# Performance work log

Hardware: AMD Instinct MI355X
Metric: run time of the kernel (lower is better)

## Reference

```python
import jax, jax.numpy as jnp
import numpy as np
from jax import lax

EPS = 1e-5


def _poly_ste(x):
    # polynomial STE: forward sign(x), backward piecewise-polynomial surrogate
    s = jnp.sign(x)
    out1 = jnp.where(x < -1.0, -1.0, x * x + 2.0 * x)
    out2 = jnp.where(x < 0.0, out1, -x * x + 2.0 * x)
    out3 = jnp.where(x < 1.0, out2, 1.0)
    return lax.stop_gradient(s - out3) + out3


def _binary_conv(x, w, stride):
    # per-filter scale (detached) * sign(w), STE through clipped weights
    scale = lax.stop_gradient(jnp.mean(jnp.abs(w), axis=(1, 2, 3), keepdims=True))
    wc = jnp.clip(w, -1.0, 1.0)
    bw = lax.stop_gradient(scale * jnp.sign(w) - wc) + wc
    return lax.conv_general_dilated(
        x, bw, window_strides=(stride, stride), padding=[(1, 1), (1, 1)],
        dimension_numbers=('NCHW', 'OIHW', 'NCHW'))


def _bn_train(x, gamma, beta):
    mu = jnp.mean(x, axis=(0, 2, 3), keepdims=True)
    var = jnp.var(x, axis=(0, 2, 3), keepdims=True)  # biased, as torch BN normalization
    return gamma.reshape(1, -1, 1, 1) * (x - mu) * lax.rsqrt(var + EPS) + beta.reshape(1, -1, 1, 1)


def _prelu(x, a):
    a = a.reshape(1, -1, 1, 1)
    return jnp.where(x >= 0, x, a * x)


def setup_inputs() -> dict:
    key = jax.random.key(0)
    ks = jax.random.split(key, 16)
    N, C, H, W = 64, 256, 28, 28
    P = 256  # planes
    d = {}
    d['x'] = jax.random.normal(ks[0], (N, C, H, W), jnp.float32)
    # LearnableBias params (init zeros in torch; small random to exercise math)
    d['b10'] = jax.random.normal(ks[1], (1, C, 1, 1), jnp.float32) * 0.01
    d['w1'] = jax.random.uniform(ks[2], (P, C, 3, 3), jnp.float32) * 0.001
    d['gamma1'] = 1.0 + 0.1 * jax.random.normal(ks[3], (P,), jnp.float32)
    d['beta1'] = 0.1 * jax.random.normal(ks[4], (P,), jnp.float32)
    d['b11'] = jax.random.normal(ks[5], (1, P, 1, 1), jnp.float32) * 0.01
    d['a1'] = 0.25 + 0.01 * jax.random.normal(ks[6], (P,), jnp.float32)
    d['b12'] = jax.random.normal(ks[7], (1, P, 1, 1), jnp.float32) * 0.01
    d['b20'] = jax.random.normal(ks[8], (1, P, 1, 1), jnp.float32) * 0.01
    d['w2'] = jax.random.uniform(ks[9], (P, P, 3, 3), jnp.float32) * 0.001
    d['gamma2'] = 1.0 + 0.1 * jax.random.normal(ks[10], (P,), jnp.float32)
    d['beta2'] = 0.1 * jax.random.normal(ks[11], (P,), jnp.float32)
    d['b21'] = jax.random.normal(ks[12], (1, P, 1, 1), jnp.float32) * 0.01
    d['a2'] = 0.25 + 0.01 * jax.random.normal(ks[13], (P,), jnp.float32)
    d['b22'] = jax.random.normal(ks[14], (1, P, 1, 1), jnp.float32) * 0.01
    return d


def reference(x, b10, w1, gamma1, beta1, b11, a1, b12,
              b20, w2, gamma2, beta2, b21, a2, b22):
    stride = 1
    residual = x
    h = x + b10
    h = _poly_ste(h)
    h = _binary_conv(h, w1, stride)
    h = _bn_train(h, gamma1, beta1)
    h = h + residual
    h = h + b11
    h = _prelu(h, a1)
    h = h + b12
    y = h + b20
    y = _poly_ste(y)
    y = _binary_conv(y, w2, stride)
    y = _bn_train(y, gamma2, beta2)
    y = y + h
    y = y + b21
    y = _prelu(y, a2)
    y = y + b22
    return y
```

## Files before the change

### kernel.cpp

```cpp
#include <hip/hip_runtime.h>

using i32x4 = __attribute__((ext_vector_type(4))) int;

#define OFF_SCALES 0u
#define OFF_AB     4096u
#define OFF_PBUF   8192u
#define OFF_WPK1   925696u
#define OFF_WPK2   1515520u
#define OFF_SPAD   2105344u
#define OFF_COUT   16850944u

__device__ __forceinline__ char sgn8(float v) {
  return v > 0.f ? (char)1 : (v < 0.f ? (char)-1 : (char)0);
}

__global__ __launch_bounds__(256) void k_wprep2(const float* __restrict__ w1,
                                                const float* __restrict__ w2,
                                                char* __restrict__ wp1,
                                                char* __restrict__ wp2,
                                                float* __restrict__ sc) {
  int bid = blockIdx.x;
  int o = bid & 255, c = threadIdx.x;
  const float* w = (bid < 256) ? w1 : w2;
  char* wp = (bid < 256) ? wp1 : wp2;
  const float* wr = w + ((size_t)o * 256 + c) * 9;
  int base = ((c >> 6) * 16384) + ((o >> 4) * 1024) +
             (((o & 15) + (((c >> 4) & 3) << 4)) << 4) + (c & 15);
  float s = 0.f;
#pragma unroll
  for (int khw = 0; khw < 9; ++khw) {
    float v = wr[khw];
    s += fabsf(v);
    wp[khw * 65536 + base] = sgn8(v);
  }
  for (int m = 1; m < 64; m <<= 1) s += __shfl_xor(s, m);
  __shared__ float red[4];
  if ((c & 63) == 0) red[c >> 6] = s;
  __syncthreads();
  if (c == 0) sc[bid] = (red[0] + red[1] + red[2] + red[3]) * (1.f / 2304.f);
}

__global__ __launch_bounds__(512) void k_e0(const float* __restrict__ x,
                                            const float* __restrict__ b10,
                                            char* __restrict__ sp) {
  __shared__ char lds[112 * 260];
  int img = blockIdx.x / 7, y4 = blockIdx.x % 7;
  int y0 = y4 * 4;
  int t = threadIdx.x;
  int r = t & 31;
  int cb = t >> 5;
  if (r < 28) {
    int p0 = r * 4;
    for (int ci = 0; ci < 16; ++ci) {
      int c = ci * 16 + cb;
      float vb = b10[c];
      size_t off = ((size_t)(img * 256 + c) * 28 + y0) * 28 + p0;
      float4 xv = *reinterpret_cast<const float4*>(x + off);
      char* lp = &lds[p0 * 260 + c];
      lp[0]   = sgn8(xv.x + vb);
      lp[260] = sgn8(xv.y + vb);
      lp[520] = sgn8(xv.z + vb);
      lp[780] = sgn8(xv.w + vb);
    }
  }
  __syncthreads();
#pragma unroll
  for (int row = 0; row < 4; ++row) {
    size_t bse = (((size_t)img * 30 + (y0 + row + 1)) * 30 + 1) * 256;
    int* spi = (int*)(sp + bse);
    for (int q = t; q < 1792; q += 512) {
      int xo = q >> 6, c4 = (q & 63) << 2;
      spi[q] = *(const int*)&lds[(row * 28 + xo) * 260 + c4];
    }
  }
  {
    int row = t >> 7, rem = t & 127;
    int col = (rem & 1) * 29, c4w = rem >> 1;
    ((int*)&sp[(((size_t)img * 30 + (y0 + row + 1)) * 30 + col) * 256])[c4w] = 0;
  }
  if (y4 == 0)
    for (int q = t; q < 1920; q += 512)
      ((int*)&sp[(size_t)img * 230400])[q] = 0;
  if (y4 == 6)
    for (int q = t; q < 1920; q += 512)
      ((int*)&sp[(size_t)img * 230400 + 29 * 7680])[q] = 0;
}

__global__ __launch_bounds__(512, 4) void k_conv(const char* __restrict__ S,
                                                 const char* __restrict__ Wp,
                                                 short* __restrict__ C,
                                                 int* __restrict__ P) {
  __shared__ char lds[46080];
  int bid = blockIdx.x;
  int img = bid / 7;
  int yt  = bid % 7;
  int tid = threadIdx.x;
  int wave = tid >> 6, lane = tid & 63;
  int l15 = lane & 15, lg = lane >> 4;
  int y0 = yt * 4;

  const char* sb = S + (size_t)img * 230400 + (size_t)y0 * 7680;
  for (int q = tid; q < 2880; q += 512) {
    int tp = q >> 4;
    int g  = q & 15;
    int k  = (tp - 2 * (tp / 30)) & 15;
    int4 v = *reinterpret_cast<const int4*>(sb + tp * 256 + g * 16);
    *reinterpret_cast<int4*>(&lds[tp * 256 + ((g ^ k) << 4)]) = v;
  }
  __syncthreads();

  int pixtp[7];
#pragma unroll
  for (int j = 0; j < 7; ++j) {
    int p = j * 16 + l15;
    pixtp[j] = (p / 28) * 30 + (p % 28);
  }
  i32x4 acc[2][7] = {};

#pragma unroll 1
  for (int kh = 0; kh < 3; ++kh) {
#pragma unroll
    for (int kw = 0; kw < 3; ++kw) {
      int khw = kh * 3 + kw;
      int shift = kh * 30 + kw;
      int kk = (l15 + 12 * kh + kw) & 15;
      const char* ab = Wp + (size_t)khw * 65536 + (size_t)wave * 2048 + lane * 16;
#pragma unroll
      for (int cc = 0; cc < 4; ++cc) {
        i32x4 afr[2];
        afr[0] = *reinterpret_cast<const i32x4*>(ab + cc * 16384);
        afr[1] = *reinterpret_cast<const i32x4*>(ab + cc * 16384 + 1024);
        int gr = (lg + 4 * cc) ^ kk;
        i32x4 bfr[7];
#pragma unroll
        for (int j = 0; j < 7; ++j) {
          int tp = pixtp[j] + shift;
          bfr[j] = *reinterpret_cast<const i32x4*>(&lds[tp * 256 + (gr << 4)]);
        }
#pragma unroll
        for (int mi = 0; mi < 2; ++mi)
#pragma unroll
          for (int j = 0; j < 7; ++j)
            acc[mi][j] = __builtin_amdgcn_mfma_i32_16x16x64_i8(afr[mi], bfr[j], acc[mi][j], 0, 0, 0);
      }
    }
  }

  short* cb = C + (size_t)img * 200704;
#pragma unroll
  for (int mi = 0; mi < 2; ++mi) {
#pragma unroll
    for (int r = 0; r < 4; ++r) {
      int o = wave * 32 + mi * 16 + lg * 4 + r;
      int s1 = 0, s2 = 0;
#pragma unroll
      for (int j = 0; j < 7; ++j) {
        int iv = acc[mi][j][r];
        int p = j * 16 + l15;
        cb[(size_t)o * 784 + (y0 + p / 28) * 28 + (p % 28)] = (short)iv;
        s1 += iv;
        s2 += iv * iv;
      }
#pragma unroll
      for (int m = 1; m < 16; m <<= 1) {
        s1 += __shfl_xor(s1, m);
        s2 += __shfl_xor(s2, m);
      }
      if (l15 == 0) {
        P[o * 448 + bid] = s1;
        P[114688 + o * 448 + bid] = s2;
      }
    }
  }
}

__global__ __launch_bounds__(256) void k_stats2(const int* __restrict__ P,
                                                const float* __restrict__ scale,
                                                const float* __restrict__ gamma,
                                                const float* __restrict__ beta,
                                                float* __restrict__ AB) {
  int o = blockIdx.x, t = threadIdx.x;
  long long s1 = 0, s2 = 0;
  for (int q = t; q < 448; q += 256) {
    s1 += P[o * 448 + q];
    s2 += P[114688 + o * 448 + q];
  }
  for (int m = 1; m < 64; m <<= 1) {
    s1 += __shfl_xor(s1, m);
    s2 += __shfl_xor(s2, m);
  }
  __shared__ long long rs1[4], rs2[4];
  if ((t & 63) == 0) { rs1[t >> 6] = s1; rs2[t >> 6] = s2; }
  __syncthreads();
  if (t == 0) {
    long long S1 = rs1[0] + rs1[1] + rs1[2] + rs1[3];
    long long S2 = rs2[0] + rs2[1] + rs2[2] + rs2[3];
    double n  = 50176.0;
    double sc = (double)scale[o];
    double mI = (double)S1 / n;
    double vI = (double)S2 / n - mI * mI;
    double mu  = sc * mI;
    double var = sc * sc * vI;
    double rr = 1.0 / sqrt(var + 1e-5);
    double g = (double)gamma[o];
    AB[o]       = (float)(g * sc * rr);
    AB[256 + o] = (float)((double)beta[o] - g * rr * mu);
  }
}

__global__ __launch_bounds__(512) void k_e1(const short* __restrict__ c1,
                                            const float* __restrict__ x,
                                            const float* __restrict__ AB,
                                            const float* __restrict__ b11,
                                            const float* __restrict__ a1,
                                            const float* __restrict__ b12,
                                            const float* __restrict__ b20,
                                            float* __restrict__ ho,
                                            char* __restrict__ sp) {
  __shared__ char lds[112 * 260];
  int img = blockIdx.x / 7, y4 = blockIdx.x % 7;
  int y0 = y4 * 4;
  int t = threadIdx.x;
  int r = t & 31;
  int cb = t >> 5;
  if (r < 28) {
    int p0 = r * 4;
    for (int ci = 0; ci < 16; ++ci) {
      int c = ci * 16 + cb;
      float A = AB[c], B = AB[256 + c];
      float v11 = b11[c], va = a1[c], v12 = b12[c], v20 = b20[c];
      size_t off = ((size_t)(img * 256 + c) * 28 + y0) * 28 + p0;
      float4 xv = *reinterpret_cast<const float4*>(x + off);
      short4 cv = *reinterpret_cast<const short4*>(c1 + off);
      float h0 = A * (float)cv.x + B + xv.x + v11; h0 = h0 >= 0.f ? h0 : va * h0; h0 += v12;
      float h1 = A * (float)cv.y + B + xv.y + v11; h1 = h1 >= 0.f ? h1 : va * h1; h1 += v12;
      float h2 = A * (float)cv.z + B + xv.z + v11; h2 = h2 >= 0.f ? h2 : va * h2; h2 += v12;
      float h3 = A * (float)cv.w + B + xv.w + v11; h3 = h3 >= 0.f ? h3 : va * h3; h3 += v12;
      float4 hv; hv.x = h0; hv.y = h1; hv.z = h2; hv.w = h3;
      *reinterpret_cast<float4*>(ho + off) = hv;
      char* lp = &lds[p0 * 260 + c];
      lp[0]   = sgn8(h0 + v20);
      lp[260] = sgn8(h1 + v20);
      lp[520] = sgn8(h2 + v20);
      lp[780] = sgn8(h3 + v20);
    }
  }
  __syncthreads();
#pragma unroll
  for (int row = 0; row < 4; ++row) {
    size_t bse = (((size_t)img * 30 + (y0 + row + 1)) * 30 + 1) * 256;
    int* spi = (int*)(sp + bse);
    for (int q = t; q < 1792; q += 512) {
      int xo = q >> 6, c4 = (q & 63) << 2;
      spi[q] = *(const int*)&lds[(row * 28 + xo) * 260 + c4];
    }
  }
}

__global__ __launch_bounds__(256) void k_e2(const short* __restrict__ c2,
                                            const float* __restrict__ AB2,
                                            const float* __restrict__ b21,
                                            const float* __restrict__ a2,
                                            const float* __restrict__ b22,
                                            float* __restrict__ io) {
  int v = blockIdx.x * 256 + threadIdx.x;
  int c = ((v * 4) / 784) & 255;
  float A = AB2[c], B = AB2[256 + c];
  float p21 = b21[c], aa = a2[c], p22 = b22[c];
  short4 I = reinterpret_cast<const short4*>(c2)[v];
  float4 h = reinterpret_cast<const float4*>(io)[v];
  float4 r;
  float t0 = A * (float)I.x + B + h.x + p21; t0 = t0 >= 0.f ? t0 : aa * t0; r.x = t0 + p22;
  float t1 = A * (float)I.y + B + h.y + p21; t1 = t1 >= 0.f ? t1 : aa * t1; r.y = t1 + p22;
  float t2 = A * (float)I.z + B + h.z + p21; t2 = t2 >= 0.f ? t2 : aa * t2; r.z = t2 + p22;
  float t3 = A * (float)I.w + B + h.w + p21; t3 = t3 >= 0.f ? t3 : aa * t3; r.w = t3 + p22;
  reinterpret_cast<float4*>(io)[v] = r;
}

extern "C" void kernel_launch(void* const* d_in, const int* in_sizes, int n_in,
                              void* d_out, int out_size, void* d_ws, size_t ws_size,
                              hipStream_t stream) {
  const float* x      = (const float*)d_in[0];
  const float* b10    = (const float*)d_in[1];
  const float* w1     = (const float*)d_in[2];
  const float* gamma1 = (const float*)d_in[3];
  const float* beta1  = (const float*)d_in[4];
  const float* b11    = (const float*)d_in[5];
  const float* a1     = (const float*)d_in[6];
  const float* b12    = (const float*)d_in[7];
  const float* b20    = (const float*)d_in[8];
  const float* w2     = (const float*)d_in[9];
  const float* gamma2 = (const float*)d_in[10];
  const float* beta2  = (const float*)d_in[11];
  const float* b21    = (const float*)d_in[12];
  const float* a2     = (const float*)d_in[13];
  const float* b22    = (const float*)d_in[14];
  float* out = (float*)d_out;

  char* ws = (char*)d_ws;
  float* scales = (float*)(ws + OFF_SCALES);
  float* AB     = (float*)(ws + OFF_AB);
  int*   pbuf   = (int*)(ws + OFF_PBUF);
  char*  wpk1   = ws + OFF_WPK1;
  char*  wpk2   = ws + OFF_WPK2;
  char*  spad   = ws + OFF_SPAD;
  short* cout   = (short*)(ws + OFF_COUT);

  k_wprep2<<<512, 256, 0, stream>>>(w1, w2, wpk1, wpk2, scales);

  k_e0<<<448, 512, 0, stream>>>(x, b10, spad);
  k_conv<<<448, 512, 0, stream>>>(spad, wpk1, cout, pbuf);
  k_stats2<<<256, 256, 0, stream>>>(pbuf, scales, gamma1, beta1, AB);
  k_e1<<<448, 512, 0, stream>>>(cout, x, AB, b11, a1, b12, b20, out, spad);
  k_conv<<<448, 512, 0, stream>>>(spad, wpk2, cout, pbuf);
  k_stats2<<<256, 256, 0, stream>>>(pbuf, scales + 256, gamma2, beta2, AB + 512);
  k_e2<<<12544, 256, 0, stream>>>(cout, AB + 512, b21, a2, b22, out);
}
```

Baseline: 132.6 us.

## Split conv rows into 8 tiles per image and stage via direct global-to-LDS loads

The conv grid changes from 448 blocks (7 row tiles of 4 per image) to 512 blocks (4 tiles of 4 rows plus 4 tiles of 3 rows), using a templated body so the work spreads evenly across the GPU's compute units. The XOR swizzle for LDS bank conflicts moves from the conv's staging loop into the producer kernels, which write the padded sign buffer already swizzled. The conv then stages its input with global_load_lds without passing through registers. The partial-stats buffer and workspace offsets are resized to 512 partials, and the 3-row tiles leave some MFMA lanes idle by clamping pixels.

```diff
diff --git a/kernel.cpp b/kernel.cpp
--- a/kernel.cpp
+++ b/kernel.cpp
@@ -5,14 +5,15 @@
 #define OFF_SCALES 0u
 #define OFF_AB     4096u
 #define OFF_PBUF   8192u
-#define OFF_WPK1   925696u
-#define OFF_WPK2   1515520u
-#define OFF_SPAD   2105344u
-#define OFF_COUT   16850944u
+#define OFF_WPK1   1056768u
+#define OFF_WPK2   1646592u
+#define OFF_SPAD   2236416u
+#define OFF_COUT   16982016u
 
 __device__ __forceinline__ char sgn8(float v) {
   return v > 0.f ? (char)1 : (v < 0.f ? (char)-1 : (char)0);
 }
+
 
 __global__ __launch_bounds__(256) void k_wprep2(const float* __restrict__ w1,
                                                 const float* __restrict__ w2,
@@ -66,11 +67,14 @@
   __syncthreads();
 #pragma unroll
   for (int row = 0; row < 4; ++row) {
-    size_t bse = (((size_t)img * 30 + (y0 + row + 1)) * 30 + 1) * 256;
+    int rp = y0 + row + 1;
+    size_t bse = (((size_t)img * 30 + rp) * 30 + 1) * 256;
     int* spi = (int*)(sp + bse);
     for (int q = t; q < 1792; q += 512) {
-      int xo = q >> 6, c4 = (q & 63) << 2;
-      spi[q] = *(const int*)&lds[(row * 28 + xo) * 260 + c4];
+      int xo = q >> 6, ii = q & 63;
+      int k = (28 * rp + xo + 1) & 15;
+      int iw = (((ii >> 2) ^ k) << 2) | (ii & 3);
+      spi[xo * 64 + iw] = *(const int*)&lds[(row * 28 + xo) * 260 + (ii << 2)];
     }
   }
   {
@@ -86,92 +90,105 @@
       ((int*)&sp[(size_t)img * 230400 + 29 * 7680])[q] = 0;
 }
 
+template<int NJ, int NPX>
+__device__ __forceinline__ void conv_body(const char* __restrict__ Wp,
+                                          short* __restrict__ cb,
+                                          int* __restrict__ P,
+                                          const char* lds,
+                                          int wave, int lane, int y0,
+                                          int ybias, int bid) {
+  int l15 = lane & 15, lg = lane >> 4;
+  int pixtp[NJ];
+#pragma unroll
+  for (int j = 0; j < NJ; ++j) {
+    int p = j * 16 + l15;
+    int pc = p < NPX ? p : NPX - 1;
+    pixtp[j] = (pc / 28) * 30 + (pc % 28);
+  }
+  i32x4 acc[2][NJ] = {};
+#pragma unroll 1
+  for (int kh = 0; kh < 3; ++kh) {
+#pragma unroll
+    for (int kw = 0; kw < 3; ++kw) {
+      int shift = kh * 30 + kw;
+      int kk = (ybias + l15 + 12 * kh + kw) & 15;
+      const char* ab = Wp + (size_t)(kh * 3 + kw) * 65536 + (size_t)wave * 2048 + lane * 16;
+#pragma unroll
+      for (int cc = 0; cc < 4; ++cc) {
+        i32x4 afr[2];
+        afr[0] = *reinterpret_cast<const i32x4*>(ab + cc * 16384);
+        afr[1] = *reinterpret_cast<const i32x4*>(ab + cc * 16384 + 1024);
+        int gr = (lg + 4 * cc) ^ kk;
+        i32x4 bfr[NJ];
+#pragma unroll
+        for (int j = 0; j < NJ; ++j)
+          bfr[j] = *reinterpret_cast<const i32x4*>(&lds[(pixtp[j] + shift) * 256 + (gr << 4)]);
+#pragma unroll
+        for (int mi = 0; mi < 2; ++mi)
+#pragma unroll
+          for (int j = 0; j < NJ; ++j)
+            acc[mi][j] = __builtin_amdgcn_mfma_i32_16x16x64_i8(afr[mi], bfr[j], acc[mi][j], 0, 0, 0);
+      }
+    }
+  }
+#pragma unroll
+  for (int mi = 0; mi < 2; ++mi) {
+#pragma unroll
+    for (int r = 0; r < 4; ++r) {
+      int o = wave * 32 + mi * 16 + lg * 4 + r;
+      int s1 = 0, s2 = 0;
+#pragma unroll
+      for (int j = 0; j < NJ; ++j) {
+        int p = j * 16 + l15;
+        if (p < NPX) {
+          int iv = acc[mi][j][r];
+          cb[(size_t)o * 784 + (y0 + p / 28) * 28 + (p % 28)] = (short)iv;
+          s1 += iv;
+          s2 += iv * iv;
+        }
+      }
+#pragma unroll
+      for (int m = 1; m < 16; m <<= 1) {
+        s1 += __shfl_xor(s1, m);
+        s2 += __shfl_xor(s2, m);
+      }
+      if (l15 == 0) {
+        P[o * 512 + bid] = s1;
+        P[131072 + o * 512 + bid] = s2;
+      }
+    }
+  }
+}
+
 __global__ __launch_bounds__(512, 4) void k_conv(const char* __restrict__ S,
                                                  const char* __restrict__ Wp,
                                                  short* __restrict__ C,
                                                  int* __restrict__ P) {
   __shared__ char lds[46080];
   int bid = blockIdx.x;
-  int img = bid / 7;
-  int yt  = bid % 7;
+  int img = bid >> 3;
+  int yt  = bid & 7;
+  int four = yt < 4;
+  int y0   = four ? yt * 4 : 16 + (yt - 4) * 3;
+  int nstg = four ? 2880 : 2400;
   int tid = threadIdx.x;
   int wave = tid >> 6, lane = tid & 63;
-  int l15 = lane & 15, lg = lane >> 4;
-  int y0 = yt * 4;
 
   const char* sb = S + (size_t)img * 230400 + (size_t)y0 * 7680;
-  for (int q = tid; q < 2880; q += 512) {
-    int tp = q >> 4;
-    int g  = q & 15;
-    int k  = (tp - 2 * (tp / 30)) & 15;
-    int4 v = *reinterpret_cast<const int4*>(sb + tp * 256 + g * 16);
-    *reinterpret_cast<int4*>(&lds[tp * 256 + ((g ^ k) << 4)]) = v;
-  }
-  __syncthreads();
-
-  int pixtp[7];
-#pragma unroll
-  for (int j = 0; j < 7; ++j) {
-    int p = j * 16 + l15;
-    pixtp[j] = (p / 28) * 30 + (p % 28);
-  }
-  i32x4 acc[2][7] = {};
-
-#pragma unroll 1
-  for (int kh = 0; kh < 3; ++kh) {
-#pragma unroll
-    for (int kw = 0; kw < 3; ++kw) {
-      int khw = kh * 3 + kw;
-      int shift = kh * 30 + kw;
-      int kk = (l15 + 12 * kh + kw) & 15;
-      const char* ab = Wp + (size_t)khw * 65536 + (size_t)wave * 2048 + lane * 16;
-#pragma unroll
-      for (int cc = 0; cc < 4; ++cc) {
-        i32x4 afr[2];
-        afr[0] = *reinterpret_cast<const i32x4*>(ab + cc * 16384);
-        afr[1] = *reinterpret_cast<const i32x4*>(ab + cc * 16384 + 1024);
-        int gr = (lg + 4 * cc) ^ kk;
-        i32x4 bfr[7];
-#pragma unroll
-        for (int j = 0; j < 7; ++j) {
-          int tp = pixtp[j] + shift;
-          bfr[j] = *reinterpret_cast<const i32x4*>(&lds[tp * 256 + (gr << 4)]);
-        }
-#pragma unroll
-        for (int mi = 0; mi < 2; ++mi)
-#pragma unroll
-          for (int j = 0; j < 7; ++j)
-            acc[mi][j] = __builtin_amdgcn_mfma_i32_16x16x64_i8(afr[mi], bfr[j], acc[mi][j], 0, 0, 0);
-      }
-    }
-  }
+  for (int q = tid; q < nstg; q += 512) {
+    int wq = q & ~63;
+    __builtin_amdgcn_global_load_lds(
+        (const __attribute__((address_space(1))) void*)(sb + (size_t)q * 16),
+        (__attribute__((address_space(3))) void*)&lds[wq * 16], 16, 0, 0);
+  }
+  __syncthreads();
 
   short* cb = C + (size_t)img * 200704;
-#pragma unroll
-  for (int mi = 0; mi < 2; ++mi) {
-#pragma unroll
-    for (int r = 0; r < 4; ++r) {
-      int o = wave * 32 + mi * 16 + lg * 4 + r;
-      int s1 = 0, s2 = 0;
-#pragma unroll
-      for (int j = 0; j < 7; ++j) {
-        int iv = acc[mi][j][r];
-        int p = j * 16 + l15;
-        cb[(size_t)o * 784 + (y0 + p / 28) * 28 + (p % 28)] = (short)iv;
-        s1 += iv;
-        s2 += iv * iv;
-      }
-#pragma unroll
-      for (int m = 1; m < 16; m <<= 1) {
-        s1 += __shfl_xor(s1, m);
-        s2 += __shfl_xor(s2, m);
-      }
-      if (l15 == 0) {
-        P[o * 448 + bid] = s1;
-        P[114688 + o * 448 + bid] = s2;
-      }
-    }
-  }
+  int ybias = (12 * y0) & 15;
+  if (four)
+    conv_body<7, 112>(Wp, cb, P, lds, wave, lane, y0, ybias, bid);
+  else
+    conv_body<6, 84>(Wp, cb, P, lds, wave, lane, y0, ybias, bid);
 }
 
 __global__ __launch_bounds__(256) void k_stats2(const int* __restrict__ P,
@@ -181,9 +198,9 @@
                                                 float* __restrict__ AB) {
   int o = blockIdx.x, t = threadIdx.x;
   long long s1 = 0, s2 = 0;
-  for (int q = t; q < 448; q += 256) {
-    s1 += P[o * 448 + q];
-    s2 += P[114688 + o * 448 + q];
+  for (int q = t; q < 512; q += 256) {
+    s1 += P[o * 512 + q];
+    s2 += P[131072 + o * 512 + q];
   }
   for (int m = 1; m < 64; m <<= 1) {
     s1 += __shfl_xor(s1, m);
@@ -248,11 +265,14 @@
   __syncthreads();
 #pragma unroll
   for (int row = 0; row < 4; ++row) {
-    size_t bse = (((size_t)img * 30 + (y0 + row + 1)) * 30 + 1) * 256;
+    int rp = y0 + row + 1;
+    size_t bse = (((size_t)img * 30 + rp) * 30 + 1) * 256;
     int* spi = (int*)(sp + bse);
     for (int q = t; q < 1792; q += 512) {
-      int xo = q >> 6, c4 = (q & 63) << 2;
-      spi[q] = *(const int*)&lds[(row * 28 + xo) * 260 + c4];
+      int xo = q >> 6, ii = q & 63;
+      int k = (28 * rp + xo + 1) & 15;
+      int iw = (((ii >> 2) ^ k) << 2) | (ii & 3);
+      spi[xo * 64 + iw] = *(const int*)&lds[(row * 28 + xo) * 260 + (ii << 2)];
     }
   }
 }
@@ -309,10 +329,10 @@
   k_wprep2<<<512, 256, 0, stream>>>(w1, w2, wpk1, wpk2, scales);
 
   k_e0<<<448, 512, 0, stream>>>(x, b10, spad);
-  k_conv<<<448, 512, 0, stream>>>(spad, wpk1, cout, pbuf);
+  k_conv<<<512, 512, 0, stream>>>(spad, wpk1, cout, pbuf);
   k_stats2<<<256, 256, 0, stream>>>(pbuf, scales, gamma1, beta1, AB);
   k_e1<<<448, 512, 0, stream>>>(cout, x, AB, b11, a1, b12, b20, out, spad);
-  k_conv<<<448, 512, 0, stream>>>(spad, wpk2, cout, pbuf);
+  k_conv<<<512, 512, 0, stream>>>(spad, wpk2, cout, pbuf);
   k_stats2<<<256, 256, 0, stream>>>(pbuf, scales + 256, gamma2, beta2, AB + 512);
   k_e2<<<12544, 256, 0, stream>>>(cout, AB + 512, b21, a2, b22, out);
 }
```

Result: no change. 134.3 us (+1.3%).

## Switch binary conv to 32x32x32 int8 MFMA, two images per block, direct-to-LDS loads

Applied to the files above, without the earlier changes.

The conv kernel now uses 32x32x32 int8 MFMA tiles instead of 16x16x64, with each block handling two images (one per group of four waves) and half as many blocks. The swizzle that was applied while staging activations into LDS is now applied by the producer kernels when they write the padded sign buffer. This lets the conv stage its tile with global_load_lds and skip the register round trip. Weight packing is reordered to match the new fragment layout. The block now uses twice the LDS and has a lower occupancy hint, and lanes for padded pixels past 112 do wasted MFMA work.

```diff
diff --git a/kernel.cpp b/kernel.cpp
--- a/kernel.cpp
+++ b/kernel.cpp
@@ -1,6 +1,7 @@
 #include <hip/hip_runtime.h>
 
-using i32x4 = __attribute__((ext_vector_type(4))) int;
+using i32x4  = __attribute__((ext_vector_type(4))) int;
+using i32x16 = __attribute__((ext_vector_type(16))) int;
 
 #define OFF_SCALES 0u
 #define OFF_AB     4096u
@@ -24,8 +25,8 @@
   const float* w = (bid < 256) ? w1 : w2;
   char* wp = (bid < 256) ? wp1 : wp2;
   const float* wr = w + ((size_t)o * 256 + c) * 9;
-  int base = ((c >> 6) * 16384) + ((o >> 4) * 1024) +
-             (((o & 15) + (((c >> 4) & 3) << 4)) << 4) + (c & 15);
+  int lane = (o & 31) | (((c >> 4) & 1) << 5);
+  int base = ((c >> 5) << 13) + ((o >> 5) << 10) + (lane << 4) + (c & 15);
   float s = 0.f;
 #pragma unroll
   for (int khw = 0; khw < 9; ++khw) {
@@ -66,11 +67,14 @@
   __syncthreads();
 #pragma unroll
   for (int row = 0; row < 4; ++row) {
-    size_t bse = (((size_t)img * 30 + (y0 + row + 1)) * 30 + 1) * 256;
+    int rp = y0 + row + 1;
+    size_t bse = (((size_t)img * 30 + rp) * 30 + 1) * 256;
     int* spi = (int*)(sp + bse);
     for (int q = t; q < 1792; q += 512) {
-      int xo = q >> 6, c4 = (q & 63) << 2;
-      spi[q] = *(const int*)&lds[(row * 28 + xo) * 260 + c4];
+      int xo = q >> 6, ii = q & 63;
+      int k = (28 * rp + xo + 1) & 15;
+      int iw = (((ii >> 2) ^ k) << 2) | (ii & 3);
+      spi[xo * 64 + iw] = *(const int*)&lds[(row * 28 + xo) * 260 + (ii << 2)];
     }
   }
   {
@@ -86,89 +90,91 @@
       ((int*)&sp[(size_t)img * 230400 + 29 * 7680])[q] = 0;
 }
 
-__global__ __launch_bounds__(512, 4) void k_conv(const char* __restrict__ S,
+__global__ __launch_bounds__(512, 2) void k_conv(const char* __restrict__ S,
                                                  const char* __restrict__ Wp,
                                                  short* __restrict__ C,
                                                  int* __restrict__ P) {
-  __shared__ char lds[46080];
+  __shared__ char lds[92160];
   int bid = blockIdx.x;
-  int img = bid / 7;
-  int yt  = bid % 7;
+  int ip = bid / 7, yt = bid % 7;
+  int img2 = ip * 2;
+  int y0 = yt * 4;
   int tid = threadIdx.x;
   int wave = tid >> 6, lane = tid & 63;
-  int l15 = lane & 15, lg = lane >> 4;
-  int y0 = yt * 4;
-
-  const char* sb = S + (size_t)img * 230400 + (size_t)y0 * 7680;
-  for (int q = tid; q < 2880; q += 512) {
-    int tp = q >> 4;
-    int g  = q & 15;
-    int k  = (tp - 2 * (tp / 30)) & 15;
-    int4 v = *reinterpret_cast<const int4*>(sb + tp * 256 + g * 16);
-    *reinterpret_cast<int4*>(&lds[tp * 256 + ((g ^ k) << 4)]) = v;
-  }
-  __syncthreads();
-
-  int pixtp[7];
-#pragma unroll
-  for (int j = 0; j < 7; ++j) {
-    int p = j * 16 + l15;
-    pixtp[j] = (p / 28) * 30 + (p % 28);
-  }
-  i32x4 acc[2][7] = {};
+  int l15 = lane & 15, l31 = lane & 31, lhi = lane >> 5;
+  int chg = wave & 3, imgh = wave >> 2;
+
+  const char* sb0 = S + (size_t)img2 * 230400 + (size_t)y0 * 7680;
+  for (int q0 = tid; q0 < 5760; q0 += 512) {
+    int half = q0 >= 2880;
+    const char* src = sb0 + (size_t)half * 230400 + (size_t)(q0 - half * 2880) * 16;
+    __builtin_amdgcn_global_load_lds(
+        (const __attribute__((address_space(1))) void*)src,
+        (__attribute__((address_space(3))) void*)&lds[(q0 & ~63) * 16], 16, 0, 0);
+  }
+  __syncthreads();
+
+  const char* ldsb = lds + imgh * 46080;
+  int pixtp[4];
+#pragma unroll
+  for (int j = 0; j < 4; ++j) {
+    int p = j * 32 + l31;
+    int pc = p < 112 ? p : 111;
+    pixtp[j] = (pc / 28) * 30 + (pc % 28);
+  }
+  i32x16 acc[2][4] = {};
+  int ybias = (12 * y0) & 15;
 
 #pragma unroll 1
   for (int kh = 0; kh < 3; ++kh) {
 #pragma unroll
     for (int kw = 0; kw < 3; ++kw) {
-      int khw = kh * 3 + kw;
       int shift = kh * 30 + kw;
-      int kk = (l15 + 12 * kh + kw) & 15;
-      const char* ab = Wp + (size_t)khw * 65536 + (size_t)wave * 2048 + lane * 16;
-#pragma unroll
-      for (int cc = 0; cc < 4; ++cc) {
-        i32x4 afr[2];
-        afr[0] = *reinterpret_cast<const i32x4*>(ab + cc * 16384);
-        afr[1] = *reinterpret_cast<const i32x4*>(ab + cc * 16384 + 1024);
-        int gr = (lg + 4 * cc) ^ kk;
-        i32x4 bfr[7];
-#pragma unroll
-        for (int j = 0; j < 7; ++j) {
-          int tp = pixtp[j] + shift;
-          bfr[j] = *reinterpret_cast<const i32x4*>(&lds[tp * 256 + (gr << 4)]);
+      int kk = (ybias + l15 + 12 * kh + kw) & 15;
+      const char* ab = Wp + (size_t)(kh * 3 + kw) * 65536 + chg * 2048 + lane * 16;
+#pragma unroll
+      for (int cc = 0; cc < 8; ++cc) {
+        i32x4 afr0 = *reinterpret_cast<const i32x4*>(ab + cc * 8192);
+        i32x4 afr1 = *reinterpret_cast<const i32x4*>(ab + cc * 8192 + 1024);
+        int gr = (cc * 2 + lhi) ^ kk;
+        i32x4 bfr[4];
+#pragma unroll
+        for (int j = 0; j < 4; ++j)
+          bfr[j] = *reinterpret_cast<const i32x4*>(&ldsb[(pixtp[j] + shift) * 256 + (gr << 4)]);
+#pragma unroll
+        for (int j = 0; j < 4; ++j) {
+          acc[0][j] = __builtin_amdgcn_mfma_i32_32x32x32_i8(afr0, bfr[j], acc[0][j], 0, 0, 0);
+          acc[1][j] = __builtin_amdgcn_mfma_i32_32x32x32_i8(afr1, bfr[j], acc[1][j], 0, 0, 0);
         }
-#pragma unroll
-        for (int mi = 0; mi < 2; ++mi)
-#pragma unroll
-          for (int j = 0; j < 7; ++j)
-            acc[mi][j] = __builtin_amdgcn_mfma_i32_16x16x64_i8(afr[mi], bfr[j], acc[mi][j], 0, 0, 0);
       }
     }
   }
 
-  short* cb = C + (size_t)img * 200704;
+  short* cb = C + (size_t)(img2 + imgh) * 200704;
 #pragma unroll
   for (int mi = 0; mi < 2; ++mi) {
 #pragma unroll
-    for (int r = 0; r < 4; ++r) {
-      int o = wave * 32 + mi * 16 + lg * 4 + r;
+    for (int reg = 0; reg < 16; ++reg) {
+      int o = chg * 64 + mi * 32 + (reg & 3) + ((reg >> 2) << 3) + (lhi << 2);
       int s1 = 0, s2 = 0;
 #pragma unroll
-      for (int j = 0; j < 7; ++j) {
-        int iv = acc[mi][j][r];
-        int p = j * 16 + l15;
-        cb[(size_t)o * 784 + (y0 + p / 28) * 28 + (p % 28)] = (short)iv;
-        s1 += iv;
-        s2 += iv * iv;
+      for (int j = 0; j < 4; ++j) {
+        int px = j * 32 + l31;
+        if (px < 112) {
+          int v = acc[mi][j][reg];
+          cb[(size_t)o * 784 + (y0 + px / 28) * 28 + (px % 28)] = (short)v;
+          s1 += v;
+          s2 += v * v;
+        }
       }
 #pragma unroll
-      for (int m = 1; m < 16; m <<= 1) {
+      for (int m = 1; m < 32; m <<= 1) {
         s1 += __shfl_xor(s1, m);
         s2 += __shfl_xor(s2, m);
       }
-      if (l15 == 0) {
-        P[o * 448 + bid] = s1;
-        P[114688 + o * 448 + bid] = s2;
+      if (l31 == 0) {
+        P[o * 448 + bid * 2 + imgh] = s1;
+        P[114688 + o * 448 + bid * 2 + imgh] = s2;
       }
     }
   }
@@ -248,11 +254,14 @@
   __syncthreads();
 #pragma unroll
   for (int row = 0; row < 4; ++row) {
-    size_t bse = (((size_t)img * 30 + (y0 + row + 1)) * 30 + 1) * 256;
+    int rp = y0 + row + 1;
+    size_t bse = (((size_t)img * 30 + rp) * 30 + 1) * 256;
     int* spi = (int*)(sp + bse);
     for (int q = t; q < 1792; q += 512) {
-      int xo = q >> 6, c4 = (q & 63) << 2;
-      spi[q] = *(const int*)&lds[(row * 28 + xo) * 260 + c4];
+      int xo = q >> 6, ii = q & 63;
+      int k = (28 * rp + xo + 1) & 15;
+      int iw = (((ii >> 2) ^ k) << 2) | (ii & 3);
+      spi[xo * 64 + iw] = *(const int*)&lds[(row * 28 + xo) * 260 + (ii << 2)];
     }
   }
 }
@@ -309,10 +318,10 @@
   k_wprep2<<<512, 256, 0, stream>>>(w1, w2, wpk1, wpk2, scales);
 
   k_e0<<<448, 512, 0, stream>>>(x, b10, spad);
-  k_conv<<<448, 512, 0, stream>>>(spad, wpk1, cout, pbuf);
+  k_conv<<<224, 512, 0, stream>>>(spad, wpk1, cout, pbuf);
   k_stats2<<<256, 256, 0, stream>>>(pbuf, scales, gamma1, beta1, AB);
   k_e1<<<448, 512, 0, stream>>>(cout, x, AB, b11, a1, b12, b20, out, spad);
-  k_conv<<<448, 512, 0, stream>>>(spad, wpk2, cout, pbuf);
+  k_conv<<<224, 512, 0, stream>>>(spad, wpk2, cout, pbuf);
   k_stats2<<<256, 256, 0, stream>>>(pbuf, scales + 256, gamma2, beta2, AB + 512);
   k_e2<<<12544, 256, 0, stream>>>(cout, AB + 512, b21, a2, b22, out);
 }
```

New measurement: 166.8 us. 25.8% more time.
